# Kernel tuning notes

Hardware: AMD Instinct MI355X
Metric: run time of the kernel (lower is better)

The kernel has to match this reference:

```python
import jax, jax.numpy as jnp
import numpy as np

B, S, E = 2, 2048, 1024          # batch, seq, emb_size
H, D = 16, 64                     # heads, head_dim
NE, K = 8, 2                      # num_experts, top_k


def setup_inputs() -> dict:
    key = jax.random.key(0)
    ks = jax.random.split(key, 12)
    w = lambda k, shape: jax.random.normal(k, shape, jnp.float32) * 0.02
    return {
        "x": jax.random.normal(ks[0], (B, S, E), jnp.float32),
        "q_w": w(ks[1], (E, E)), "q_b": jnp.zeros((E,), jnp.float32),
        "k_w": w(ks[2], (E, E)), "k_b": jnp.zeros((E,), jnp.float32),
        "v_w": w(ks[3], (E, E)), "v_b": jnp.zeros((E,), jnp.float32),
        "gate_w": w(ks[4], (NE, E)), "gate_b": jnp.zeros((NE,), jnp.float32),
        "expert_w": w(ks[5], (NE, E, E)), "expert_b": jnp.zeros((NE, E), jnp.float32),
        "ffn_w": w(ks[6], (E, E)), "ffn_b": jnp.zeros((E,), jnp.float32),
    }


def _rope_cos_sin(seq_len, dim):
    inv_freq = 1.0 / (10000.0 ** (jnp.arange(0, dim, 2, dtype=jnp.float32) / dim))
    freqs = jnp.outer(jnp.arange(seq_len, dtype=jnp.float32), inv_freq)  # [S, D/2]
    emb = jnp.concatenate([freqs, freqs], axis=-1)                        # [S, D]
    return jnp.cos(emb), jnp.sin(emb)


def _rotate_half(x):
    x1, x2 = jnp.split(x, 2, axis=-1)
    return jnp.concatenate([-x2, x1], axis=-1)


def reference(x, q_w, q_b, k_w, k_b, v_w, v_b, gate_w, gate_b, expert_w, expert_b, ffn_w, ffn_b):
    b, s, _ = x.shape
    q = (x @ q_w.T + q_b).reshape(b, s, H, D)
    k = (x @ k_w.T + k_b).reshape(b, s, H, D)
    v = (x @ v_w.T + v_b).reshape(b, s, H, D)

    cos, sin = _rope_cos_sin(s, D)          # [S, D]
    cos = cos[None, :, None, :]
    sin = sin[None, :, None, :]
    q = q * cos + _rotate_half(q) * sin
    k = k * cos + _rotate_half(k) * sin

    # full (memory-efficient-style) attention, scale 1/sqrt(D)
    scores = jnp.einsum('bqhd,bkhd->bhqk', q, k) / jnp.sqrt(jnp.float32(D))
    attn = jax.nn.softmax(scores, axis=-1)
    attn_out = jnp.einsum('bhqk,bkhd->bqhd', attn, v).reshape(b, s, E)

    # MoE: dense-compute all experts, gather top-k, weighted combine
    gates = jax.nn.softmax(attn_out @ gate_w.T + gate_b, axis=-1)        # [B,S,NE]
    top_gates, top_idx = jax.lax.top_k(gates, K)                          # [B,S,K]
    # Linear per expert: y = x W^T + b,  expert_w: [NE, out, in]
    expert_outputs = jnp.einsum('bsi,noi->bsno', attn_out, expert_w) + expert_b  # [B,S,NE,E]
    sel = jnp.take_along_axis(expert_outputs, top_idx[..., None], axis=2)        # [B,S,K,E]
    moe_out = jnp.einsum('bsk,bskh->bsh', top_gates, sel)                        # [B,S,E]

    # dropout is identity at inference; ffn + residual
    return moe_out @ ffn_w.T + ffn_b + x
```

## Files before the change

kernel.cpp:

```cpp
#include <hip/hip_runtime.h>
#include <hip/hip_bf16.h>

#define B_ 2
#define S_ 2048
#define E_ 1024
#define H_ 16
#define D_ 64
#define NE_ 8
#define TOKENS (B_*S_)

typedef __attribute__((ext_vector_type(8))) short bf16x8;
typedef __attribute__((ext_vector_type(4))) float f32x4;
typedef unsigned short u16;
typedef unsigned int u32;

__device__ __forceinline__ u16 f2bf(float f) {
    u32 u = __float_as_uint(f);
    u32 r = u + 0x7fffu + ((u >> 16) & 1u);
    return (u16)(r >> 16);
}
__device__ __forceinline__ float bf2f(u16 h) {
    return __uint_as_float(((u32)h) << 16);
}
__device__ __forceinline__ void gl2lds16(const void* g, void* l) {
    __builtin_amdgcn_global_load_lds(
        (__attribute__((address_space(1))) void*)(g),
        (__attribute__((address_space(3))) void*)(l), 16, 0, 0);
}
#define MFMA16(a,b,c) __builtin_amdgcn_mfma_f32_16x16x32_bf16(a,b,c,0,0,0)

__global__ void cvt_all_k(
    const float* __restrict__ x,  const float* __restrict__ qw,
    const float* __restrict__ kw, const float* __restrict__ vw,
    const float* __restrict__ fw, const float* __restrict__ ew,
    u16* __restrict__ xh,  u16* __restrict__ qwh, u16* __restrict__ kwh,
    u16* __restrict__ vwh, u16* __restrict__ fwh, u16* __restrict__ ewh)
{
    const int blk = blockIdx.x;
    const float* s; u16* d; int off;
    if (blk < 4096)      { s = x;  d = xh;  off = blk; }
    else if (blk < 5120) { s = qw; d = qwh; off = blk - 4096; }
    else if (blk < 6144) { s = kw; d = kwh; off = blk - 5120; }
    else if (blk < 7168) { s = vw; d = vwh; off = blk - 6144; }
    else if (blk < 8192) { s = fw; d = fwh; off = blk - 7168; }
    else                 { s = ew; d = ewh; off = blk - 8192; }
    const size_t i = (size_t)off * 256 + threadIdx.x;
    const float4 v = *(const float4*)(s + i * 4);
    ushort4 H = {f2bf(v.x), f2bf(v.y), f2bf(v.z), f2bf(v.w)};
    *(ushort4*)(d + i * 4) = H;
}

__global__ void rope_tab_kernel(float2* __restrict__ tab)
{
    const int idx = blockIdx.x * 256 + threadIdx.x;
    const int s = idx >> 5, d1 = idx & 31;
    const float inv = exp2f(-(float)d1 * 0.41524101186091903f);
    float sn, cs;
    sincosf((float)s * inv, &sn, &cs);
    tab[idx] = make_float2(cs, sn);
}

__global__ __launch_bounds__(256,2) void gemm_qkv(
    const u16* __restrict__ Ah,
    const u16* __restrict__ qwh, const u16* __restrict__ kwh,
    const u16* __restrict__ vwh,
    const float* __restrict__ q_b, const float* __restrict__ k_b,
    const float* __restrict__ v_b,
    const float2* __restrict__ tab,
    u16* __restrict__ Qhb, u16* __restrict__ Khb, u16* __restrict__ Vtb)
{
    __shared__ __align__(16) u16 sA[128*32], sB[128*32];
    const int z = blockIdx.z;
    const u16* Bh = (z == 0) ? qwh : (z == 1) ? kwh : vwh;
    const float* bias = (z == 0) ? q_b : (z == 1) ? k_b : v_b;
    const int t = threadIdx.x;
    const int m0 = blockIdx.y * 128, n0 = blockIdx.x * 128;
    const int lane = t & 63, w = t >> 6;
    const int wm = w >> 1, wn = w & 1;
    const int lr = lane & 15, qd = lane >> 4;
    f32x4 acc[4][4] = {};
    const size_t gA = (size_t)(m0 + (t >> 2)) * E_ + (t & 3) * 8;
    const size_t gB = (size_t)(n0 + (t >> 2)) * E_ + (t & 3) * 8;
    for (int k0 = 0; k0 < E_; k0 += 32) {
        #pragma unroll
        for (int is = 0; is < 2; is++) {
            const int ldo = (is * 256 + (t & 192)) * 16;
            const size_t ro = (size_t)is * 64 * E_;
            gl2lds16(Ah + gA + ro + k0, (char*)sA + ldo);
            gl2lds16(Bh + gB + ro + k0, (char*)sB + ldo);
        }
        __syncthreads();
        bf16x8 af[4], bfr[4];
        #pragma unroll
        for (int i = 0; i < 4; i++) {
            af[i]  = *(const bf16x8*)&sA[(wm*64 + i*16 + lr)*32 + qd*8];
            bfr[i] = *(const bf16x8*)&sB[(wn*64 + i*16 + lr)*32 + qd*8];
        }
        #pragma unroll
        for (int i = 0; i < 4; i++)
            #pragma unroll
            for (int j = 0; j < 4; j++)
                acc[i][j] = MFMA16(af[i], bfr[j], acc[i][j]);
        __syncthreads();
    }
    const int head = (n0 + wn * 64) >> 6;
    if (z < 2) {
        u16* Oh = (z == 0) ? Qhb : Khb;
        #pragma unroll
        for (int j = 0; j < 2; j++) {
            const int d1 = j * 16 + lr;
            const float b1 = bias[head * 64 + d1];
            const float b2 = bias[head * 64 + d1 + 32];
            #pragma unroll
            for (int i = 0; i < 4; i++) {
                #pragma unroll
                for (int r = 0; r < 4; r++) {
                    const int tok = m0 + wm*64 + i*16 + qd*4 + r;
                    const int bb = tok >> 11, ss = tok & (S_ - 1);
                    const float2 t2 = tab[ss * 32 + d1];
                    const float q1 = acc[i][j][r]   + b1;
                    const float q2 = acc[i][j+2][r] + b2;
                    const size_t o = (((size_t)bb * H_ + head) * S_ + ss) * 64 + d1;
                    Oh[o]    = f2bf(q1 * t2.x - q2 * t2.y);
                    Oh[o+32] = f2bf(q2 * t2.x + q1 * t2.y);
                }
            }
        }
    } else {
        #pragma unroll
        for (int j = 0; j < 4; j++) {
            const int d = j * 16 + lr;
            const float bv = bias[head * 64 + d];
            #pragma unroll
            for (int i = 0; i < 4; i++)
                #pragma unroll
                for (int r = 0; r < 4; r++) {
                    const int tok = m0 + wm*64 + i*16 + qd*4 + r;
                    const int bb = tok >> 11, ss = tok & (S_ - 1);
                    Vtb[(((size_t)bb * H_ + head) * 64 + d) * S_ + ss] = f2bf(acc[i][j][r] + bv);
                }
        }
    }
}

__global__ __launch_bounds__(256,4) void attn_kernel(
    const u16* __restrict__ Q, const u16* __restrict__ K,
    const u16* __restrict__ Vt,
    u16* __restrict__ attn_bf, float* __restrict__ attn_f32)
{
    __shared__ __align__(16) u16 sK[64*64];
    __shared__ __align__(16) u16 sV[64*64];
    __shared__ __align__(16) u16 sP[4][16*40];
    const int t = threadIdx.x, lane = t & 63, w = t >> 6;
    const int lr = lane & 15, qd = lane >> 4;
    const int q0 = blockIdx.x * 64;
    const int h = blockIdx.y, b = blockIdx.z;
    const size_t bhS = ((size_t)b * H_ + h) * S_;
    const size_t bhD = ((size_t)b * H_ + h) * 64;
    bf16x8 qf0, qf1;
    {
        const size_t qa = (bhS + q0 + w * 16 + lr) * 64 + qd * 8;
        qf0 = *(const bf16x8*)&Q[qa];
        qf1 = *(const bf16x8*)&Q[qa + 32];
    }
    f32x4 O[4] = {};
    float lsum[4] = {};
    for (int j0 = 0; j0 < S_; j0 += 64) {
        #pragma unroll
        for (int it = 0; it < 2; it++) {
            const int CH = (it*4 + w)*4 + qd;
            const int sbs = CH >> 3;
            const int doff = ((CH >> 2) & 1)*32 + (CH & 3)*8;
            gl2lds16(&K [(bhS + j0 + sbs*16 + lr)*64 + doff],
                     (char*)sK + (it*4 + w)*1024);
            gl2lds16(&Vt[(bhD + sbs*16 + lr)*S_ + j0 + doff],
                     (char*)sV + (it*4 + w)*1024);
        }
        __syncthreads();
        f32x4 Sv[4];
        #pragma unroll
        for (int sb = 0; sb < 4; sb++) {
            bf16x8 k0 = *(const bf16x8*)&sK[(sb*8 + qd)*128 + lr*8];
            bf16x8 k1 = *(const bf16x8*)&sK[(sb*8 + 4 + qd)*128 + lr*8];
            f32x4 a = {};
            a = MFMA16(qf0, k0, a);
            a = MFMA16(qf1, k1, a);
            Sv[sb] = a;
        }
        float ps[4] = {};
        #pragma unroll
        for (int sb = 0; sb < 4; sb++)
            #pragma unroll
            for (int r = 0; r < 4; r++) {
                const float pv = __expf(Sv[sb][r] * 0.125f);
                ps[r] += pv;
                sP[w][(qd*4 + r)*40 + sb*16 + lr] = f2bf(pv);
            }
        #pragma unroll
        for (int r = 0; r < 4; r++) lsum[r] += ps[r];
        bf16x8 p0 = *(const bf16x8*)&sP[w][lr*40 + qd*8];
        bf16x8 p1 = *(const bf16x8*)&sP[w][lr*40 + 32 + qd*8];
        #pragma unroll
        for (int ds = 0; ds < 4; ds++) {
            bf16x8 v0 = *(const bf16x8*)&sV[(ds*8 + qd)*128 + lr*8];
            bf16x8 v1 = *(const bf16x8*)&sV[(ds*8 + 4 + qd)*128 + lr*8];
            O[ds] = MFMA16(p0, v0, O[ds]);
            O[ds] = MFMA16(p1, v1, O[ds]);
        }
        __syncthreads();
    }
    float linv[4];
    #pragma unroll
    for (int r = 0; r < 4; r++) {
        float s2 = lsum[r];
        s2 += __shfl_xor(s2, 1, 64);
        s2 += __shfl_xor(s2, 2, 64);
        s2 += __shfl_xor(s2, 4, 64);
        s2 += __shfl_xor(s2, 8, 64);
        linv[r] = 1.f / s2;
    }
    #pragma unroll
    for (int ds = 0; ds < 4; ds++)
        #pragma unroll
        for (int r = 0; r < 4; r++) {
            const int q = q0 + w * 16 + qd * 4 + r;
            const size_t o = (size_t)(b*S_ + q)*E_ + h*64 + ds*16 + lr;
            const float val = O[ds][r] * linv[r];
            attn_bf[o]  = f2bf(val);
            attn_f32[o] = val;
        }
}

__global__ __launch_bounds__(256) void gate_topk_kernel(
    const float* __restrict__ attn_f32, const float* __restrict__ gate_w,
    const float* __restrict__ gate_b, float* __restrict__ gval,
    int* __restrict__ eidx)
{
    const int t = threadIdx.x;
    const int token = blockIdx.x * 4 + (t >> 6);
    const int lane  = t & 63;
    const float* a = attn_f32 + (size_t)token * E_;
    float part[NE_] = {};
    for (int i = lane; i < E_; i += 64) {
        const float av = a[i];
        #pragma unroll
        for (int n = 0; n < NE_; n++) part[n] += av * gate_w[n*E_ + i];
    }
    #pragma unroll
    for (int n = 0; n < NE_; n++) {
        #pragma unroll
        for (int off = 32; off >= 1; off >>= 1)
            part[n] += __shfl_down(part[n], off, 64);
    }
    if (lane == 0) {
        float lg[NE_];
        #pragma unroll
        for (int n = 0; n < NE_; n++) lg[n] = part[n] + gate_b[n];
        float m = lg[0];
        #pragma unroll
        for (int n = 1; n < NE_; n++) m = fmaxf(m, lg[n]);
        float ex[NE_], ssum = 0.f;
        #pragma unroll
        for (int n = 0; n < NE_; n++) { ex[n] = __expf(lg[n]-m); ssum += ex[n]; }
        const float invs = 1.f / ssum;
        int i0 = 0;
        #pragma unroll
        for (int n = 1; n < NE_; n++) if (lg[n] > lg[i0]) i0 = n;
        int i1 = (i0 == 0) ? 1 : 0;
        #pragma unroll
        for (int n = 0; n < NE_; n++) if (n != i0 && lg[n] > lg[i1]) i1 = n;
        eidx[token*2]     = i0;
        gval[token*2]     = ex[i0]*invs;
        eidx[token*2 + 1] = i1;
        gval[token*2 + 1] = ex[i1]*invs;
    }
}

__global__ __launch_bounds__(256) void build_lists_kernel(
    const int* __restrict__ eidx, int* __restrict__ list, int* __restrict__ counts)
{
    __shared__ int lcnt[NE_], lbase[NE_];
    const int t = threadIdx.x;
    if (t < NE_) lcnt[t] = 0;
    __syncthreads();
    const int ent = blockIdx.x * 512 + t * 2;
    const int e0 = eidx[ent], e1 = eidx[ent + 1];
    const int p0 = atomicAdd(&lcnt[e0], 1);
    const int p1 = atomicAdd(&lcnt[e1], 1);
    __syncthreads();
    if (t < NE_) lbase[t] = atomicAdd(&counts[t], lcnt[t]);
    __syncthreads();
    list[e0 * TOKENS + lbase[e0] + p0] = ent;
    list[e1 * TOKENS + lbase[e1] + p1] = ent + 1;
}

__global__ __launch_bounds__(256,2) void gemm_expert(
    const u16* __restrict__ Abf, const u16* __restrict__ ewh,
    const float* __restrict__ eb, const int* __restrict__ list,
    const int* __restrict__ counts, const float* __restrict__ gval,
    u16* __restrict__ sel)
{
    const int e = blockIdx.z;
    const int cnt = counts[e];
    const int m0 = blockIdx.y * 128;
    if (m0 >= cnt) return;
    __shared__ __align__(16) u16 sA[128*32], sB[128*32];
    __shared__ int sEnt[128];
    const int t = threadIdx.x;
    if (t < 128) sEnt[t] = (m0 + t < cnt) ? list[e * TOKENS + m0 + t] : -1;
    __syncthreads();
    const int n0 = blockIdx.x * 128;
    const int lane = t & 63, w = t >> 6;
    const int wm = w >> 1, wn = w & 1;
    const int lr = lane & 15, qd = lane >> 4;
    const int e0 = sEnt[t >> 2], e1 = sEnt[64 + (t >> 2)];
    const u16* ga0 = Abf + (size_t)(e0 < 0 ? 0 : (e0 >> 1)) * E_ + (t & 3) * 8;
    const u16* ga1 = Abf + (size_t)(e1 < 0 ? 0 : (e1 >> 1)) * E_ + (t & 3) * 8;
    const u16* gb0 = ewh + (size_t)e * E_ * E_ + (size_t)(n0 + (t >> 2)) * E_ + (t & 3) * 8;
    const u16* gb1 = gb0 + 64 * E_;
    f32x4 acc[4][4] = {};
    for (int k0 = 0; k0 < E_; k0 += 32) {
        {
            const int l0 = (t & 192) * 16;
            const int l1 = (256 + (t & 192)) * 16;
            gl2lds16(ga0 + k0, (char*)sA + l0);
            gl2lds16(ga1 + k0, (char*)sA + l1);
            gl2lds16(gb0 + k0, (char*)sB + l0);
            gl2lds16(gb1 + k0, (char*)sB + l1);
        }
        __syncthreads();
        bf16x8 af[4], bfr[4];
        #pragma unroll
        for (int i = 0; i < 4; i++) {
            af[i]  = *(const bf16x8*)&sA[(wm*64 + i*16 + lr)*32 + qd*8];
            bfr[i] = *(const bf16x8*)&sB[(wn*64 + i*16 + lr)*32 + qd*8];
        }
        #pragma unroll
        for (int i = 0; i < 4; i++)
            #pragma unroll
            for (int j = 0; j < 4; j++)
                acc[i][j] = MFMA16(af[i], bfr[j], acc[i][j]);
        __syncthreads();
    }
    #pragma unroll
    for (int i = 0; i < 4; i++)
        #pragma unroll
        for (int r = 0; r < 4; r++) {
            const int local = wm*64 + i*16 + qd*4 + r;
            const int ent = sEnt[local];
            if (ent < 0) continue;
            const float g = gval[ent];
            #pragma unroll
            for (int j = 0; j < 4; j++) {
                const int col = n0 + wn*64 + j*16 + lr;
                sel[(size_t)ent * E_ + col] = f2bf((acc[i][j][r] + eb[e * E_ + col]) * g);
            }
        }
}

__global__ void combine_kernel(const u16* __restrict__ sel, u16* __restrict__ moe)
{
    const int g = blockIdx.x * 256 + threadIdx.x;
    const int tok = g >> 8;
    const int c = (g & 255) * 4;
    const u16* a = sel + (size_t)tok * 2048 + c;
    float o[4];
    #pragma unroll
    for (int j = 0; j < 4; j++) o[j] = bf2f(a[j]) + bf2f(a[1024 + j]);
    ushort4 R = {f2bf(o[0]), f2bf(o[1]), f2bf(o[2]), f2bf(o[3])};
    *(ushort4*)(moe + (size_t)tok * E_ + c) = R;
}

__global__ __launch_bounds__(256,2) void gemm_ffn(
    const u16* __restrict__ Ah, const u16* __restrict__ Bh,
    const float* __restrict__ bias, const float* __restrict__ res,
    float* __restrict__ C)
{
    __shared__ __align__(16) u16 sA[128*32], sB[128*32];
    const int t = threadIdx.x;
    const int m0 = blockIdx.y * 128, n0 = blockIdx.x * 128;
    const int lane = t & 63, w = t >> 6;
    const int wm = w >> 1, wn = w & 1;
    const int lr = lane & 15, qd = lane >> 4;
    f32x4 acc[4][4] = {};
    const size_t gA = (size_t)(m0 + (t >> 2)) * E_ + (t & 3) * 8;
    const size_t gB = (size_t)(n0 + (t >> 2)) * E_ + (t & 3) * 8;
    for (int k0 = 0; k0 < E_; k0 += 32) {
        #pragma unroll
        for (int is = 0; is < 2; is++) {
            const int ldo = (is * 256 + (t & 192)) * 16;
            const size_t ro = (size_t)is * 64 * E_;
            gl2lds16(Ah + gA + ro + k0, (char*)sA + ldo);
            gl2lds16(Bh + gB + ro + k0, (char*)sB + ldo);
        }
        __syncthreads();
        bf16x8 af[4], bfr[4];
        #pragma unroll
        for (int i = 0; i < 4; i++) {
            af[i]  = *(const bf16x8*)&sA[(wm*64 + i*16 + lr)*32 + qd*8];
            bfr[i] = *(const bf16x8*)&sB[(wn*64 + i*16 + lr)*32 + qd*8];
        }
        #pragma unroll
        for (int i = 0; i < 4; i++)
            #pragma unroll
            for (int j = 0; j < 4; j++)
                acc[i][j] = MFMA16(af[i], bfr[j], acc[i][j]);
        __syncthreads();
    }
    #pragma unroll
    for (int i = 0; i < 4; i++)
        #pragma unroll
        for (int r = 0; r < 4; r++) {
            const int tok = m0 + wm*64 + i*16 + qd*4 + r;
            #pragma unroll
            for (int j = 0; j < 4; j++) {
                const int col = n0 + wn*64 + j*16 + lr;
                C[(size_t)tok * E_ + col] = acc[i][j][r] + bias[col] + res[(size_t)tok * E_ + col];
            }
        }
}

extern "C" void kernel_launch(void* const* d_in, const int* in_sizes, int n_in,
                              void* d_out, int out_size, void* d_ws, size_t ws_size,
                              hipStream_t stream) {
    const float* x      = (const float*)d_in[0];
    const float* q_w    = (const float*)d_in[1];
    const float* q_b    = (const float*)d_in[2];
    const float* k_w    = (const float*)d_in[3];
    const float* k_b    = (const float*)d_in[4];
    const float* v_w    = (const float*)d_in[5];
    const float* v_b    = (const float*)d_in[6];
    const float* gate_w = (const float*)d_in[7];
    const float* gate_b = (const float*)d_in[8];
    const float* ew     = (const float*)d_in[9];
    const float* eb     = (const float*)d_in[10];
    const float* ffn_w  = (const float*)d_in[11];
    const float* ffn_b  = (const float*)d_in[12];
    float* out = (float*)d_out;

    char* p = (char*)d_ws;
    auto alloc = [&](size_t bytes) { char* r = p; p += (bytes + 255) & ~(size_t)255; return r; };
    u16* xh   = (u16*)alloc((size_t)TOKENS*E_*2);
    u16* qwh  = (u16*)alloc((size_t)E_*E_*2);
    u16* kwh  = (u16*)alloc((size_t)E_*E_*2);
    u16* vwh  = (u16*)alloc((size_t)E_*E_*2);
    u16* fwh  = (u16*)alloc((size_t)E_*E_*2);
    u16* ewh  = (u16*)alloc((size_t)NE_*E_*E_*2);
    u16* Qhb  = (u16*)alloc((size_t)TOKENS*E_*2);
    u16* Khb  = (u16*)alloc((size_t)TOKENS*E_*2);
    u16* Vtb  = (u16*)alloc((size_t)TOKENS*E_*2);
    u16* abf  = (u16*)alloc((size_t)TOKENS*E_*2);
    float* af32 = (float*)alloc((size_t)TOKENS*E_*4);
    u16* selb = (u16*)alloc((size_t)2*TOKENS*E_*2);
    u16* moeb = (u16*)alloc((size_t)TOKENS*E_*2);
    float2* rtab = (float2*)alloc((size_t)S_*32*8);
    float* gvl = (float*)alloc((size_t)2*TOKENS*4);
    int*   eix = (int*)alloc((size_t)2*TOKENS*4);
    int*   lst = (int*)alloc((size_t)NE_*TOKENS*4);
    int*   cnt = (int*)alloc(256);

    hipMemsetAsync(cnt, 0, 256, stream);

    rope_tab_kernel<<<S_*32/256, 256, 0, stream>>>(rtab);
    cvt_all_k<<<16384, 256, 0, stream>>>(x, q_w, k_w, v_w, ffn_w, ew,
                                         xh, qwh, kwh, vwh, fwh, ewh);

    gemm_qkv<<<dim3(8,32,3), 256, 0, stream>>>(xh, qwh, kwh, vwh,
                                               q_b, k_b, v_b, rtab,
                                               Qhb, Khb, Vtb);

    attn_kernel<<<dim3(32,16,2), 256, 0, stream>>>(Qhb, Khb, Vtb, abf, af32);

    gate_topk_kernel<<<TOKENS/4, 256, 0, stream>>>(af32, gate_w, gate_b, gvl, eix);
    build_lists_kernel<<<TOKENS/256, 256, 0, stream>>>(eix, lst, cnt);
    gemm_expert<<<dim3(8,32,8), 256, 0, stream>>>(abf, ewh, eb, lst, cnt, gvl, selb);
    combine_kernel<<<4096, 256, 0, stream>>>(selb, moeb);
    gemm_ffn<<<dim3(8,32), 256, 0, stream>>>(moeb, fwh, ffn_b, x, out);
}
```

Measured before the change: 317.9 us.

## Split attention over KV halves, double query tile, fuse combine with gating

Each attention block now handles 128 queries, two 64-row sub-tiles sharing every loaded K/V tile, and only half of the key sequence (split-K). This doubles reuse of staged K/V and keeps the grid size unchanged. Unnormalized partial outputs and row sums go to fp32 buffers. A new per-token kernel sums the two partials, normalizes, writes the bf16 activations and computes the gate softmax and top-2, replacing the old gate kernel and the fp32 attention copy. It costs extra fp32 partial traffic (two TOKENS×E arrays) and more registers per thread in the attention kernel.

```diff
diff --git a/kernel.cpp b/kernel.cpp
--- a/kernel.cpp
+++ b/kernel.cpp
@@ -146,26 +146,29 @@
 __global__ __launch_bounds__(256,4) void attn_kernel(
     const u16* __restrict__ Q, const u16* __restrict__ K,
     const u16* __restrict__ Vt,
-    u16* __restrict__ attn_bf, float* __restrict__ attn_f32)
+    float* __restrict__ Opart, float* __restrict__ lpart)
 {
     __shared__ __align__(16) u16 sK[64*64];
     __shared__ __align__(16) u16 sV[64*64];
-    __shared__ __align__(16) u16 sP[4][16*40];
+    __shared__ __align__(16) u16 sP[4][2][16*40];
     const int t = threadIdx.x, lane = t & 63, w = t >> 6;
     const int lr = lane & 15, qd = lane >> 4;
-    const int q0 = blockIdx.x * 64;
-    const int h = blockIdx.y, b = blockIdx.z;
+    const int q0 = blockIdx.x * 128;
+    const int h = blockIdx.y;
+    const int b = blockIdx.z & 1, sc = blockIdx.z >> 1;
     const size_t bhS = ((size_t)b * H_ + h) * S_;
     const size_t bhD = ((size_t)b * H_ + h) * 64;
-    bf16x8 qf0, qf1;
-    {
-        const size_t qa = (bhS + q0 + w * 16 + lr) * 64 + qd * 8;
-        qf0 = *(const bf16x8*)&Q[qa];
-        qf1 = *(const bf16x8*)&Q[qa + 32];
-    }
-    f32x4 O[4] = {};
-    float lsum[4] = {};
-    for (int j0 = 0; j0 < S_; j0 += 64) {
+    bf16x8 qf[2][2];
+    #pragma unroll
+    for (int p = 0; p < 2; p++) {
+        const size_t qa = (bhS + q0 + p*64 + w*16 + lr) * 64 + qd * 8;
+        qf[p][0] = *(const bf16x8*)&Q[qa];
+        qf[p][1] = *(const bf16x8*)&Q[qa + 32];
+    }
+    f32x4 O[2][4] = {};
+    float lsum[2][4] = {};
+    const int jbeg = sc * 1024, jend = jbeg + 1024;
+    for (int j0 = jbeg; j0 < jend; j0 += 64) {
         #pragma unroll
         for (int it = 0; it < 2; it++) {
             const int CH = (it*4 + w)*4 + qd;
@@ -177,102 +180,142 @@
                      (char*)sV + (it*4 + w)*1024);
         }
         __syncthreads();
-        f32x4 Sv[4];
-        #pragma unroll
-        for (int sb = 0; sb < 4; sb++) {
-            bf16x8 k0 = *(const bf16x8*)&sK[(sb*8 + qd)*128 + lr*8];
-            bf16x8 k1 = *(const bf16x8*)&sK[(sb*8 + 4 + qd)*128 + lr*8];
-            f32x4 a = {};
-            a = MFMA16(qf0, k0, a);
-            a = MFMA16(qf1, k1, a);
-            Sv[sb] = a;
-        }
-        float ps[4] = {};
-        #pragma unroll
-        for (int sb = 0; sb < 4; sb++)
-            #pragma unroll
-            for (int r = 0; r < 4; r++) {
-                const float pv = __expf(Sv[sb][r] * 0.125f);
-                ps[r] += pv;
-                sP[w][(qd*4 + r)*40 + sb*16 + lr] = f2bf(pv);
-            }
-        #pragma unroll
-        for (int r = 0; r < 4; r++) lsum[r] += ps[r];
-        bf16x8 p0 = *(const bf16x8*)&sP[w][lr*40 + qd*8];
-        bf16x8 p1 = *(const bf16x8*)&sP[w][lr*40 + 32 + qd*8];
-        #pragma unroll
-        for (int ds = 0; ds < 4; ds++) {
-            bf16x8 v0 = *(const bf16x8*)&sV[(ds*8 + qd)*128 + lr*8];
-            bf16x8 v1 = *(const bf16x8*)&sV[(ds*8 + 4 + qd)*128 + lr*8];
-            O[ds] = MFMA16(p0, v0, O[ds]);
-            O[ds] = MFMA16(p1, v1, O[ds]);
-        }
-        __syncthreads();
-    }
-    float linv[4];
-    #pragma unroll
-    for (int r = 0; r < 4; r++) {
-        float s2 = lsum[r];
-        s2 += __shfl_xor(s2, 1, 64);
-        s2 += __shfl_xor(s2, 2, 64);
-        s2 += __shfl_xor(s2, 4, 64);
-        s2 += __shfl_xor(s2, 8, 64);
-        linv[r] = 1.f / s2;
-    }
-    #pragma unroll
-    for (int ds = 0; ds < 4; ds++)
+        {
+            f32x4 Sv[2][4];
+            #pragma unroll
+            for (int sb = 0; sb < 4; sb++) {
+                bf16x8 k0 = *(const bf16x8*)&sK[(sb*8 + qd)*128 + lr*8];
+                bf16x8 k1 = *(const bf16x8*)&sK[(sb*8 + 4 + qd)*128 + lr*8];
+                f32x4 a0 = {}, a1 = {};
+                a0 = MFMA16(qf[0][0], k0, a0);
+                a0 = MFMA16(qf[0][1], k1, a0);
+                a1 = MFMA16(qf[1][0], k0, a1);
+                a1 = MFMA16(qf[1][1], k1, a1);
+                Sv[0][sb] = a0;
+                Sv[1][sb] = a1;
+            }
+            #pragma unroll
+            for (int p = 0; p < 2; p++) {
+                float ps[4] = {};
+                #pragma unroll
+                for (int sb = 0; sb < 4; sb++)
+                    #pragma unroll
+                    for (int r = 0; r < 4; r++) {
+                        const float pv = __expf(Sv[p][sb][r] * 0.125f);
+                        ps[r] += pv;
+                        sP[w][p][(qd*4 + r)*40 + sb*16 + lr] = f2bf(pv);
+                    }
+                #pragma unroll
+                for (int r = 0; r < 4; r++) lsum[p][r] += ps[r];
+            }
+        }
+        {
+            bf16x8 vv[8];
+            #pragma unroll
+            for (int ds = 0; ds < 4; ds++) {
+                vv[2*ds]   = *(const bf16x8*)&sV[(ds*8 + qd)*128 + lr*8];
+                vv[2*ds+1] = *(const bf16x8*)&sV[(ds*8 + 4 + qd)*128 + lr*8];
+            }
+            #pragma unroll
+            for (int p = 0; p < 2; p++) {
+                bf16x8 p0 = *(const bf16x8*)&sP[w][p][lr*40 + qd*8];
+                bf16x8 p1 = *(const bf16x8*)&sP[w][p][lr*40 + 32 + qd*8];
+                #pragma unroll
+                for (int ds = 0; ds < 4; ds++) {
+                    O[p][ds] = MFMA16(p0, vv[2*ds],   O[p][ds]);
+                    O[p][ds] = MFMA16(p1, vv[2*ds+1], O[p][ds]);
+                }
+            }
+        }
+        __syncthreads();
+    }
+    float* Op = Opart + (size_t)sc * TOKENS * E_;
+    float* lp = lpart + (size_t)sc * TOKENS * H_;
+    #pragma unroll
+    for (int p = 0; p < 2; p++) {
         #pragma unroll
         for (int r = 0; r < 4; r++) {
-            const int q = q0 + w * 16 + qd * 4 + r;
-            const size_t o = (size_t)(b*S_ + q)*E_ + h*64 + ds*16 + lr;
-            const float val = O[ds][r] * linv[r];
-            attn_bf[o]  = f2bf(val);
-            attn_f32[o] = val;
-        }
-}
-
-__global__ __launch_bounds__(256) void gate_topk_kernel(
-    const float* __restrict__ attn_f32, const float* __restrict__ gate_w,
-    const float* __restrict__ gate_b, float* __restrict__ gval,
-    int* __restrict__ eidx)
-{
+            float s2 = lsum[p][r];
+            s2 += __shfl_xor(s2, 1, 64);
+            s2 += __shfl_xor(s2, 2, 64);
+            s2 += __shfl_xor(s2, 4, 64);
+            s2 += __shfl_xor(s2, 8, 64);
+            lsum[p][r] = s2;
+        }
+        const int qb = q0 + p*64 + w*16 + qd*4;
+        if (lr == 0) {
+            #pragma unroll
+            for (int r = 0; r < 4; r++)
+                lp[(size_t)(b*S_ + qb + r) * H_ + h] = lsum[p][r];
+        }
+        #pragma unroll
+        for (int ds = 0; ds < 4; ds++)
+            #pragma unroll
+            for (int r = 0; r < 4; r++)
+                Op[(size_t)(b*S_ + qb + r) * E_ + h*64 + ds*16 + lr] = O[p][ds][r];
+    }
+}
+
+__global__ __launch_bounds__(256) void combine_gate(
+    const float* __restrict__ Opart, const float* __restrict__ lpart,
+    const float* __restrict__ gate_w, const float* __restrict__ gate_b,
+    u16* __restrict__ attn_bf, float* __restrict__ gval, int* __restrict__ eidx)
+{
+    __shared__ float red[4][NE_];
+    __shared__ float lg8[NE_];
+    const int tok = blockIdx.x;
     const int t = threadIdx.x;
-    const int token = blockIdx.x * 4 + (t >> 6);
-    const int lane  = t & 63;
-    const float* a = attn_f32 + (size_t)token * E_;
-    float part[NE_] = {};
-    for (int i = lane; i < E_; i += 64) {
-        const float av = a[i];
-        #pragma unroll
-        for (int n = 0; n < NE_; n++) part[n] += av * gate_w[n*E_ + i];
-    }
-    #pragma unroll
-    for (int n = 0; n < NE_; n++) {
+    const int d4 = t * 4;
+    const int h = d4 >> 6;
+    const float l = lpart[(size_t)tok*H_ + h] + lpart[(size_t)(TOKENS + tok)*H_ + h];
+    const float inv = 1.f / l;
+    const float4 o1 = *(const float4*)&Opart[(size_t)tok*E_ + d4];
+    const float4 o2 = *(const float4*)&Opart[(size_t)(TOKENS + tok)*E_ + d4];
+    float v[4] = {(o1.x+o2.x)*inv, (o1.y+o2.y)*inv, (o1.z+o2.z)*inv, (o1.w+o2.w)*inv};
+    ushort4 H4 = {f2bf(v[0]), f2bf(v[1]), f2bf(v[2]), f2bf(v[3])};
+    *(ushort4*)&attn_bf[(size_t)tok*E_ + d4] = H4;
+    float pe[NE_];
+    #pragma unroll
+    for (int e = 0; e < NE_; e++) {
+        const float4 g = *(const float4*)&gate_w[e*E_ + d4];
+        pe[e] = v[0]*g.x + v[1]*g.y + v[2]*g.z + v[3]*g.w;
+    }
+    #pragma unroll
+    for (int e = 0; e < NE_; e++) {
         #pragma unroll
         for (int off = 32; off >= 1; off >>= 1)
-            part[n] += __shfl_down(part[n], off, 64);
-    }
-    if (lane == 0) {
+            pe[e] += __shfl_xor(pe[e], off, 64);
+    }
+    const int w = t >> 6;
+    if ((t & 63) == 0) {
+        #pragma unroll
+        for (int e = 0; e < NE_; e++) red[w][e] = pe[e];
+    }
+    __syncthreads();
+    if (t < NE_)
+        lg8[t] = red[0][t] + red[1][t] + red[2][t] + red[3][t] + gate_b[t];
+    __syncthreads();
+    if (t == 0) {
         float lg[NE_];
         #pragma unroll
-        for (int n = 0; n < NE_; n++) lg[n] = part[n] + gate_b[n];
+        for (int e = 0; e < NE_; e++) lg[e] = lg8[e];
         float m = lg[0];
         #pragma unroll
-        for (int n = 1; n < NE_; n++) m = fmaxf(m, lg[n]);
+        for (int e = 1; e < NE_; e++) m = fmaxf(m, lg[e]);
         float ex[NE_], ssum = 0.f;
         #pragma unroll
-        for (int n = 0; n < NE_; n++) { ex[n] = __expf(lg[n]-m); ssum += ex[n]; }
+        for (int e = 0; e < NE_; e++) { ex[e] = __expf(lg[e]-m); ssum += ex[e]; }
         const float invs = 1.f / ssum;
         int i0 = 0;
         #pragma unroll
-        for (int n = 1; n < NE_; n++) if (lg[n] > lg[i0]) i0 = n;
+        for (int e = 1; e < NE_; e++) if (lg[e] > lg[i0]) i0 = e;
         int i1 = (i0 == 0) ? 1 : 0;
         #pragma unroll
-        for (int n = 0; n < NE_; n++) if (n != i0 && lg[n] > lg[i1]) i1 = n;
-        eidx[token*2]     = i0;
-        gval[token*2]     = ex[i0]*invs;
-        eidx[token*2 + 1] = i1;
-        gval[token*2 + 1] = ex[i1]*invs;
+        for (int e = 0; e < NE_; e++) if (e != i0 && lg[e] > lg[i1]) i1 = e;
+        eidx[tok*2]     = i0;
+        gval[tok*2]     = ex[i0]*invs;
+        eidx[tok*2 + 1] = i1;
+        gval[tok*2 + 1] = ex[i1]*invs;
     }
 }
 
@@ -450,7 +493,8 @@
     u16* Khb  = (u16*)alloc((size_t)TOKENS*E_*2);
     u16* Vtb  = (u16*)alloc((size_t)TOKENS*E_*2);
     u16* abf  = (u16*)alloc((size_t)TOKENS*E_*2);
-    float* af32 = (float*)alloc((size_t)TOKENS*E_*4);
+    float* Opart = (float*)alloc((size_t)2*TOKENS*E_*4);
+    float* lpart = (float*)alloc((size_t)2*TOKENS*H_*4);
     u16* selb = (u16*)alloc((size_t)2*TOKENS*E_*2);
     u16* moeb = (u16*)alloc((size_t)TOKENS*E_*2);
     float2* rtab = (float2*)alloc((size_t)S_*32*8);
@@ -469,9 +513,10 @@
                                                q_b, k_b, v_b, rtab,
                                                Qhb, Khb, Vtb);
 
-    attn_kernel<<<dim3(32,16,2), 256, 0, stream>>>(Qhb, Khb, Vtb, abf, af32);
-
-    gate_topk_kernel<<<TOKENS/4, 256, 0, stream>>>(af32, gate_w, gate_b, gvl, eix);
+    attn_kernel<<<dim3(16,16,4), 256, 0, stream>>>(Qhb, Khb, Vtb, Opart, lpart);
+
+    combine_gate<<<TOKENS, 256, 0, stream>>>(Opart, lpart, gate_w, gate_b,
+                                             abf, gvl, eix);
     build_lists_kernel<<<TOKENS/256, 256, 0, stream>>>(eix, lst, cnt);
     gemm_expert<<<dim3(8,32,8), 256, 0, stream>>>(abf, ewh, eb, lst, cnt, gvl, selb);
     combine_kernel<<<4096, 256, 0, stream>>>(selb, moeb);
```

Measured after the change: 304.4 us. 4.2% less time.
